# Optimization experiments

Hardware: AMD Instinct MI355X
Metric: run time of the kernel (lower is better)

The kernel has to match this reference:

```python
import jax, jax.numpy as jnp
import numpy as np

HEADS = 8
SCALE_BASE = 512
EPS = 1e-5


def xpos(x, downscale=False):
    # x: (B, h, S, hd) ; XPOS rotary embedding with exponential scale
    hd = x.shape[-1]
    S = x.shape[-2]
    half = hd // 2
    base_scale = (jnp.arange(0, hd, 2, dtype=jnp.float32) + 0.4 * hd) / (1.4 * hd)  # (half,)
    pos = jnp.arange(S, dtype=jnp.float32)
    scale = base_scale[None, :] ** (pos[:, None] / SCALE_BASE)  # (S, half)
    inv_freq = 1.0 / (10000.0 ** (jnp.arange(half, dtype=jnp.float32) / half))
    sinu = pos[:, None] * inv_freq[None, :]  # (S, half)
    sin, cos = jnp.sin(sinu), jnp.cos(sinu)
    if downscale:
        scale = 1.0 / scale
    # duplicate_interleave: (S, half) -> (S, hd)
    sin_s = jnp.repeat(sin * scale, 2, axis=-1)
    cos_s = jnp.repeat(cos * scale, 2, axis=-1)
    x1 = x[..., ::2]
    x2 = x[..., 1::2]
    rot = jnp.stack((-x2, x1), axis=-1).reshape(x.shape)  # rotate_every_two
    return x * cos_s + rot * sin_s


def decay_mask(S):
    # (heads, S, S): gamma^(n-m) for n>=m else 0
    gammas = 1.0 - jnp.exp(jnp.linspace(np.log(1 / 32), np.log(1 / 512), HEADS)).astype(jnp.float32)
    n = jnp.arange(S, dtype=jnp.float32)
    diff = n[:, None] - n[None, :]
    lg = jnp.log(gammas)[:, None, None]
    return jnp.where(diff >= 0, jnp.exp(jnp.maximum(diff, 0.0) * lg), 0.0)


def layer_norm(x, w, b):
    mu = x.mean(-1, keepdims=True)
    var = x.var(-1, keepdims=True)
    return (x - mu) / jnp.sqrt(var + EPS) * w + b


def multiscale_retention(Xq, Xkv, Wq, Wk, Wv, Wg, Wo, gn_w, gn_b):
    # Xq: (B,S,d) query source; Xkv: (B,S,d) key/value source (== Xq for self)
    B, S, _ = Xq.shape
    Q = jnp.einsum('bsd,hde->bhse', Xq, Wq)
    K = jnp.einsum('btd,hde->bhte', Xkv, Wk)
    V = jnp.einsum('btd,hdv->bhtv', Xkv, Wv)
    Q = xpos(Q)
    K = xpos(K, downscale=True)
    D = decay_mask(S)  # (h,S,S)
    scores = jnp.einsum('bhse,bhte->bhst', Q, K) * D[None]
    Y = jnp.einsum('bhst,bhtv->bhsv', scores, V)  # (B,h,S,hv)
    h, hv = Y.shape[1], Y.shape[3]
    # GroupNorm(heads, v_dim) over each head's channels per token
    mu = Y.mean(-1, keepdims=True)
    var = Y.var(-1, keepdims=True)
    Yn = (Y - mu) / jnp.sqrt(var + EPS)
    Yn = Yn.transpose(0, 2, 1, 3).reshape(B, S, h * hv) * gn_w + gn_b
    gate = jax.nn.sigmoid(Xq @ Wg) * (Xq @ Wg)  # swish gate
    return (gate * Yn) @ Wo


def setup_inputs() -> dict:
    key = jax.random.key(0)
    ks = jax.random.split(key, 32)
    d, f, h, hd, hv, vd = 1024, 4096, 8, 128, 256, 2048
    B, S = 2, 2048
    inp = {
        'X': jax.random.normal(ks[0], (B, S, d), jnp.float32),
        'mem': jax.random.normal(ks[1], (B, S, d), jnp.float32),
        'ln1_w': jax.random.uniform(ks[2], (d,), jnp.float32, 0.5, 1.5),
        'ln1_b': jax.random.normal(ks[3], (d,), jnp.float32) * 0.1,
        'ln2_w': jax.random.uniform(ks[4], (d,), jnp.float32, 0.5, 1.5),
        'ln2_b': jax.random.normal(ks[5], (d,), jnp.float32) * 0.1,
        'Wq': jax.random.normal(ks[6], (h, d, hd), jnp.float32) / d,
        'Wk': jax.random.normal(ks[7], (h, d, hd), jnp.float32) / d,
        'Wv': jax.random.normal(ks[8], (h, d, hv), jnp.float32) / d,
        'Wg': jax.random.normal(ks[9], (d, vd), jnp.float32) / d,
        'Wo': jax.random.normal(ks[10], (vd, d), jnp.float32) / d,
        'gn_w': jax.random.uniform(ks[11], (vd,), jnp.float32, 0.5, 1.5),
        'gn_b': jax.random.normal(ks[12], (vd,), jnp.float32) * 0.1,
        'cWq': jax.random.normal(ks[13], (h, d, hd), jnp.float32) / d,
        'cWk': jax.random.normal(ks[14], (h, d, hd), jnp.float32) / d,
        'cWv': jax.random.normal(ks[15], (h, d, hv), jnp.float32) / d,
        'cWg': jax.random.normal(ks[16], (d, vd), jnp.float32) / d,
        'cWo': jax.random.normal(ks[17], (vd, d), jnp.float32) / d,
        'cgn_w': jax.random.uniform(ks[18], (vd,), jnp.float32, 0.5, 1.5),
        'cgn_b': jax.random.normal(ks[19], (vd,), jnp.float32) * 0.1,
        'W1': jax.random.normal(ks[20], (d, f), jnp.float32) * (1.0 / np.sqrt(d)),
        'b1': jax.random.normal(ks[21], (f,), jnp.float32) * 0.02,
        'W2': jax.random.normal(ks[22], (f, d), jnp.float32) * (1.0 / np.sqrt(f)),
        'b2': jax.random.normal(ks[23], (d,), jnp.float32) * 0.02,
    }
    return inp


def reference(X, mem, ln1_w, ln1_b, ln2_w, ln2_b, Wq, Wk, Wv, Wg, Wo, gn_w, gn_b,
              cWq, cWk, cWv, cWg, cWo, cgn_w, cgn_b, W1, b1, W2, b2):
    # self retention block
    X = multiscale_retention(layer_norm(X, ln1_w, ln1_b), None, Wq, Wk, Wv, Wg, Wo, gn_w, gn_b) + X if False else multiscale_retention(layer_norm(X, ln1_w, ln1_b), layer_norm(X, ln1_w, ln1_b), Wq, Wk, Wv, Wg, Wo, gn_w, gn_b) + X
    # cross retention block (note: original reuses layer_norms_2 for both this and the FFN)
    h2 = layer_norm(X, ln2_w, ln2_b)
    X = multiscale_retention(h2, mem, cWq, cWk, cWv, cWg, cWo, cgn_w, cgn_b) + X
    # FFN block (GELU exact, per torch nn.GELU default)
    h3 = layer_norm(X, ln2_w, ln2_b)
    X = (jax.nn.gelu(h3 @ W1 + b1, approximate=False) @ W2 + b2) + X
    return X
```

## Files before the change

kernel.cpp:

```cpp
#include <hip/hip_runtime.h>
#include <math.h>

#define RTOT 4096
#define SEQQ 2048

typedef unsigned int uint32;
typedef __attribute__((ext_vector_type(4))) float f32x4;
typedef __attribute__((ext_vector_type(8))) short bf16x8;

__device__ __forceinline__ unsigned short f2bf(float f) {
  unsigned int u = __float_as_uint(f);
  u = (u + 0x7FFFu + ((u >> 16) & 1u)) >> 16;
  return (unsigned short)u;
}
__device__ __forceinline__ float bf2f(unsigned short h) {
  return __uint_as_float(((unsigned int)h) << 16);
}
__device__ __forceinline__ void gld16(const void* g, void* l) {
  __builtin_amdgcn_global_load_lds(
      (const __attribute__((address_space(1))) uint32*)g,
      (__attribute__((address_space(3))) uint32*)l, 16, 0, 0);
}
__device__ __forceinline__ void bar() {
  asm volatile("" ::: "memory");
  __builtin_amdgcn_s_barrier();
  asm volatile("" ::: "memory");
}
#define VMCNT(n) asm volatile("s_waitcnt vmcnt(" #n ")" ::: "memory")

__global__ __launch_bounds__(256) void transpose_bf16(
    const float* __restrict__ in, unsigned short* __restrict__ out, int R, int C,
    int perm) {
  __shared__ float t[32][33];
  int z = blockIdx.z;
  in  += (size_t)z * R * C;
  out += (size_t)z * C * R;
  int r0 = blockIdx.x * 32, c0 = blockIdx.y * 32;
  int tx = threadIdx.x & 31, ty = threadIdx.x >> 5;
  #pragma unroll
  for (int i = 0; i < 4; ++i) {
    int r = ty + i * 8;
    t[r][tx] = in[(size_t)(r0 + r) * C + c0 + tx];
  }
  __syncthreads();
  #pragma unroll
  for (int i = 0; i < 4; ++i) {
    int cc = c0 + ty + i * 8;
    if (perm) cc = 64 * (cc >> 6) + ((cc & 1) << 5) + ((cc & 63) >> 1);
    out[(size_t)cc * R + r0 + tx] = f2bf(t[tx][ty + i * 8]);
  }
}

__global__ __launch_bounds__(256) void cvt_bf16(
    const float* __restrict__ in, unsigned short* __restrict__ out, int n8) {
  int i = blockIdx.x * 256 + threadIdx.x;
  if (i >= n8) return;
  const float4* p = (const float4*)(in + (size_t)i * 8);
  float4 a = p[0], b = p[1];
  bf16x8 v;
  v[0] = (short)f2bf(a.x); v[1] = (short)f2bf(a.y); v[2] = (short)f2bf(a.z); v[3] = (short)f2bf(a.w);
  v[4] = (short)f2bf(b.x); v[5] = (short)f2bf(b.y); v[6] = (short)f2bf(b.z); v[7] = (short)f2bf(b.w);
  *(bf16x8*)(out + (size_t)i * 8) = v;
}

__global__ __launch_bounds__(256) void tabgen(float* __restrict__ tab) {
  int i = blockIdx.x * 256 + threadIdx.x;
  int pos = i >> 6, j = i & 63;
  float bs = (2.f * (float)j + 51.2f) * (1.f / 179.2f);
  float e = (float)pos * (1.f / 512.f);
  float sc = exp2f(e * log2f(bs));
  float invf = exp2f(-(float)j * (13.287712379549449f / 64.f));
  float su, cu;
  sincosf((float)pos * invf, &su, &cu);
  tab[i]            = cu * sc;
  tab[131072 + i]   = su * sc;
  float si = 1.f / sc;
  tab[262144 + i]   = cu * si;
  tab[393216 + i]   = su * si;
}

__global__ __launch_bounds__(256) void ln_bf16(const float* __restrict__ x,
    const float* __restrict__ w, const float* __restrict__ b,
    unsigned short* __restrict__ out) {
  int row = blockIdx.x, tid = threadIdx.x;
  const float* xr = x + (size_t)row * 1024;
  float4 v = *(const float4*)(xr + tid * 4);
  float s  = v.x + v.y + v.z + v.w;
  float ss = v.x*v.x + v.y*v.y + v.z*v.z + v.w*v.w;
  #pragma unroll
  for (int o = 32; o > 0; o >>= 1) { s += __shfl_down(s, o); ss += __shfl_down(ss, o); }
  __shared__ float red[2][4];
  int wid = tid >> 6;
  if ((tid & 63) == 0) { red[0][wid] = s; red[1][wid] = ss; }
  __syncthreads();
  float st  = red[0][0] + red[0][1] + red[0][2] + red[0][3];
  float sst = red[1][0] + red[1][1] + red[1][2] + red[1][3];
  float mu   = st * (1.f / 1024.f);
  float var  = sst * (1.f / 1024.f) - mu * mu;
  float rstd = rsqrtf(var + 1e-5f);
  float4 wv = *(const float4*)(w + tid * 4);
  float4 bv = *(const float4*)(b + tid * 4);
  unsigned short o0 = f2bf((v.x - mu) * rstd * wv.x + bv.x);
  unsigned short o1 = f2bf((v.y - mu) * rstd * wv.y + bv.y);
  unsigned short o2 = f2bf((v.z - mu) * rstd * wv.z + bv.z);
  unsigned short o3 = f2bf((v.w - mu) * rstd * wv.w + bv.w);
  ushort4 o4 = make_ushort4(o0, o1, o2, o3);
  *(ushort4*)(out + (size_t)row * 1024 + tid * 4) = o4;
}

enum { EPI_F32_RES = 0, EPI_BF16 = 1, EPI_XPOS = 2, EPI_GELU = 4, EPI_BRES = 5,
       EPI_QKG = 6, EPI_QG = 7 };

struct EpiP {
  void* C; int ldc;
  const float* bias; const float* resid;
  const float* tab;
  unsigned short* oQ; unsigned short* oK; unsigned short* oG;
};

template<int EPI>
__device__ __forceinline__ void epi_store(size_t m, int n, int N0, float v, const EpiP& P) {
  if constexpr (EPI == EPI_BF16) {
    ((unsigned short*)P.C)[m * P.ldc + n] = f2bf(v);
  } else if constexpr (EPI == EPI_GELU) {
    v += P.bias[n];
    v = 0.5f * v * (1.f + erff(v * 0.70710678f));
    ((unsigned short*)P.C)[m * P.ldc + n] = f2bf(v);
  } else if constexpr (EPI == EPI_BRES) {
    v += P.bias[n] + P.resid[m * P.ldc + n];
    ((float*)P.C)[m * P.ldc + n] = v;
  } else {
    v += P.resid[m * P.ldc + n];
    ((float*)P.C)[m * P.ldc + n] = v;
  }
}

template<int EPI>
__global__ __launch_bounds__(256) void gemm_mfma(
    const unsigned short* __restrict__ A, int lda,
    const unsigned short* __restrict__ Bt, int ldb, int K, int nbx, EpiP P) {
  __shared__ __align__(16) unsigned short As[2][128 * 32];
  __shared__ __align__(16) unsigned short Bs[2][128 * 32];
  const int tid = threadIdx.x, w = tid >> 6, lane = tid & 63;
  int q8 = (int)gridDim.x >> 3;
  int sbid = ((int)blockIdx.x & 7) * q8 + ((int)blockIdx.x >> 3);
  int by = sbid / nbx, bx = sbid - by * nbx;
  const int M0 = by * 128, N0 = bx * 128;
  const int fr = lane & 15, fs = lane >> 4;
  const int srow = lane >> 2, sp = lane & 3;

  f32x4 zf = {0.f, 0.f, 0.f, 0.f};
  f32x4 acc[4][4];
  #pragma unroll
  for (int i = 0; i < 4; ++i)
    #pragma unroll
    for (int j = 0; j < 4; ++j) acc[i][j] = zf;

  auto STAGE = [&](int buf, int k0) {
    #pragma unroll
    for (int c = 0; c < 4; ++c) {
      int ch = w * 4 + c;
      int cc = ch & 7;
      int row = cc * 16 + srow;
      int so = sp ^ ((row >> 1) & 3);
      if (ch < 8) gld16(A  + (size_t)(M0 + row) * lda + k0 + so * 8, &As[buf][cc * 512]);
      else        gld16(Bt + (size_t)(N0 + row) * ldb + k0 + so * 8, &Bs[buf][cc * 512]);
    }
  };

  STAGE(0, 0);
  int cur = 0;
  for (int k0 = 0; k0 < K; k0 += 32) {
    if (k0 + 32 < K) { STAGE(cur ^ 1, k0 + 32); VMCNT(4); }
    else             { VMCNT(0); }
    bar();
    bf16x8 af[4], bfr[4];
    #pragma unroll
    for (int mi = 0; mi < 4; ++mi) {
      int row = (w >> 1) * 64 + mi * 16 + fr;
      af[mi] = *(const bf16x8*)(&As[cur][row * 32 + (fs ^ ((row >> 1) & 3)) * 8]);
    }
    #pragma unroll
    for (int ni = 0; ni < 4; ++ni) {
      int row = (w & 1) * 64 + ni * 16 + fr;
      bfr[ni] = *(const bf16x8*)(&Bs[cur][row * 32 + (fs ^ ((row >> 1) & 3)) * 8]);
    }
    #pragma unroll
    for (int mi = 0; mi < 4; ++mi)
      #pragma unroll
      for (int ni = 0; ni < 4; ++ni)
        acc[mi][ni] = __builtin_amdgcn_mfma_f32_16x16x32_bf16(af[mi], bfr[ni], acc[mi][ni], 0, 0, 0);
    bar();
    cur ^= 1;
  }

  #pragma unroll
  for (int mi = 0; mi < 4; ++mi)
    #pragma unroll
    for (int r = 0; r < 4; ++r) {
      size_t m = M0 + (w >> 1) * 64 + mi * 16 + fs * 4 + r;
      #pragma unroll
      for (int ni = 0; ni < 4; ++ni) {
        int n = N0 + (w & 1) * 64 + ni * 16 + fr;
        epi_store<EPI>(m, n, N0, acc[mi][ni][r], P);
      }
    }
}

template<int EPI>
__global__ __launch_bounds__(256) void gemm_bn64(
    const unsigned short* __restrict__ A, int lda,
    const unsigned short* __restrict__ Bt, int ldb, int K, int nbx, EpiP P) {
  __shared__ __align__(16) unsigned short As[2][128 * 32];
  __shared__ __align__(16) unsigned short Bs[2][64 * 32];
  const int tid = threadIdx.x, w = tid >> 6, lane = tid & 63;
  int q8 = (int)gridDim.x >> 3;
  int sbid = ((int)blockIdx.x & 7) * q8 + ((int)blockIdx.x >> 3);
  int by = sbid / nbx, bx = sbid - by * nbx;
  const int M0 = by * 128, N0 = bx * 64;
  const int fr = lane & 15, fs = lane >> 4;
  const int srow = lane >> 2, sp = lane & 3;

  f32x4 zf = {0.f, 0.f, 0.f, 0.f};
  f32x4 acc[2][4];
  #pragma unroll
  for (int i = 0; i < 2; ++i)
    #pragma unroll
    for (int j = 0; j < 4; ++j) acc[i][j] = zf;

  auto STAGE = [&](int buf, int k0) {
    #pragma unroll
    for (int c = 0; c < 3; ++c) {
      int ch = w * 3 + c;
      if (ch < 8) {
        int row = ch * 16 + srow;
        int so = sp ^ ((row >> 1) & 3);
        gld16(A + (size_t)(M0 + row) * lda + k0 + so * 8, &As[buf][ch * 512]);
      } else {
        int bch = ch - 8;
        int row = bch * 16 + srow;
        int so = sp ^ ((row >> 1) & 3);
        gld16(Bt + (size_t)(N0 + row) * ldb + k0 + so * 8, &Bs[buf][bch * 512]);
      }
    }
  };

  STAGE(0, 0);
  int cur = 0;
  for (int k0 = 0; k0 < K; k0 += 32) {
    if (k0 + 32 < K) { STAGE(cur ^ 1, k0 + 32); VMCNT(3); }
    else             { VMCNT(0); }
    bar();
    bf16x8 af[2], bfr[4];
    #pragma unroll
    for (int mi = 0; mi < 2; ++mi) {
      int row = w * 32 + mi * 16 + fr;
      af[mi] = *(const bf16x8*)(&As[cur][row * 32 + (fs ^ ((row >> 1) & 3)) * 8]);
    }
    #pragma unroll
    for (int ni = 0; ni < 4; ++ni) {
      int row = ni * 16 + fr;
      bfr[ni] = *(const bf16x8*)(&Bs[cur][row * 32 + (fs ^ ((row >> 1) & 3)) * 8]);
    }
    #pragma unroll
    for (int mi = 0; mi < 2; ++mi)
      #pragma unroll
      for (int ni = 0; ni < 4; ++ni)
        acc[mi][ni] = __builtin_amdgcn_mfma_f32_16x16x32_bf16(af[mi], bfr[ni], acc[mi][ni], 0, 0, 0);
    bar();
    cur ^= 1;
  }

  if constexpr (EPI == EPI_XPOS) {
    int gsel = (N0 >> 6) & 1;
    #pragma unroll
    for (int mi = 0; mi < 2; ++mi)
      #pragma unroll
      for (int r = 0; r < 4; ++r) {
        size_t m = M0 + w * 32 + mi * 16 + fs * 4 + r;
        int pos = (int)(m & (SEQQ - 1));
        #pragma unroll
        for (int ni = 0; ni < 2; ++ni) {
          int j = gsel * 32 + ni * 16 + fr;
          float cs = P.tab[pos * 64 + j], sn = P.tab[131072 + pos * 64 + j];
          float ve = acc[mi][ni][r], vo = acc[mi][ni + 2][r];
          unsigned short* dst = (unsigned short*)P.C;
          dst[m * P.ldc + N0 + ni * 16 + fr]       = f2bf(ve * cs - vo * sn);
          dst[m * P.ldc + N0 + (ni + 2) * 16 + fr] = f2bf(vo * cs + ve * sn);
        }
      }
  } else {
    #pragma unroll
    for (int mi = 0; mi < 2; ++mi)
      #pragma unroll
      for (int r = 0; r < 4; ++r) {
        size_t m = M0 + w * 32 + mi * 16 + fs * 4 + r;
        #pragma unroll
        for (int ni = 0; ni < 4; ++ni) {
          int n = N0 + ni * 16 + fr;
          epi_store<EPI>(m, n, N0, acc[mi][ni][r], P);
        }
      }
  }
}

template<int EPI>
__global__ __launch_bounds__(512, 2) void gemm256(
    const unsigned short* __restrict__ A,
    const unsigned short* __restrict__ Bt,
    int nbx, EpiP P) {
  __shared__ __align__(16) unsigned short lds[4][2][8192];
  const int tid = threadIdx.x, w = tid >> 6, lane = tid & 63;
  int cpx = (int)gridDim.x >> 3;
  int sbid = ((int)blockIdx.x & 7) * cpx + ((int)blockIdx.x >> 3);
  int by = sbid / nbx, bx = sbid - by * nbx;
  const int M0 = by * 256, N0 = bx * 256;
  const int wm = w >> 2, wn = w & 3;
  const int fr = lane & 15, fs = lane >> 4;
  const int srow = lane >> 2;
  const int sslot = (lane & 3) ^ ((lane >> 3) & 3);
  const int rsw = (fr >> 1) & 3;

  f32x4 acc[8][4];
  #pragma unroll
  for (int i = 0; i < 8; ++i)
    #pragma unroll
    for (int j = 0; j < 4; ++j) acc[i][j] = {0.f, 0.f, 0.f, 0.f};

  auto STAGE = [&](int t, int buf) {
    int k0 = t * 32;
    #pragma unroll
    for (int j = 0; j < 4; ++j) {
      int c = w * 4 + j;
      if (c < 16)
        gld16(A  + (size_t)(M0 + c * 16 + srow) * 1024 + k0 + sslot * 8,
              &lds[buf][0][c * 512]);
      else
        gld16(Bt + (size_t)(N0 + (c - 16) * 16 + srow) * 1024 + k0 + sslot * 8,
              &lds[buf][1][(c - 16) * 512]);
    }
  };
  auto COMPUTE = [&](int t) {
    const unsigned short* la = &lds[t & 3][0][wm * 128 * 32];
    const unsigned short* lb = &lds[t & 3][1][wn * 64 * 32];
    bf16x8 a[8], b[4];
    #pragma unroll
    for (int ni = 0; ni < 4; ++ni)
      b[ni] = *(const bf16x8*)(lb + (ni * 16 + fr) * 32 + ((fs ^ rsw) * 8));
    #pragma unroll
    for (int mi = 0; mi < 8; ++mi)
      a[mi] = *(const bf16x8*)(la + (mi * 16 + fr) * 32 + ((fs ^ rsw) * 8));
    #pragma unroll
    for (int mi = 0; mi < 8; ++mi)
      #pragma unroll
      for (int ni = 0; ni < 4; ++ni)
        acc[mi][ni] = __builtin_amdgcn_mfma_f32_16x16x32_bf16(a[mi], b[ni], acc[mi][ni], 0, 0, 0);
  };

  STAGE(0, 0); STAGE(1, 1); STAGE(2, 2);
  for (int t = 0; t < 29; ++t) {
    STAGE(t + 3, (t + 3) & 3);
    VMCNT(12);
    bar();
    COMPUTE(t);
    bar();
  }
  VMCNT(8);  bar(); COMPUTE(29); bar();
  VMCNT(4);  bar(); COMPUTE(30); bar();
  VMCNT(0);  bar(); COMPUTE(31);

  if constexpr (EPI == EPI_GELU) {
    #pragma unroll
    for (int mi = 0; mi < 8; ++mi)
      #pragma unroll
      for (int r = 0; r < 4; ++r) {
        size_t m = M0 + wm * 128 + mi * 16 + fs * 4 + r;
        #pragma unroll
        for (int ni = 0; ni < 4; ++ni) {
          int n = N0 + wn * 64 + ni * 16 + fr;
          float v = acc[mi][ni][r] + P.bias[n];
          v = 0.5f * v * (1.f + erff(v * 0.70710678f));
          ((unsigned short*)P.C)[m * P.ldc + n] = f2bf(v);
        }
      }
  } else {
    const int nb = N0 + wn * 64;
    const bool isQ = nb < 1024;
    const bool isK = (EPI == EPI_QKG) && !isQ && (nb < 2048);
    if (isQ || isK) {
      const float* tc = isK ? P.tab + 262144 : P.tab;
      const float* ts = tc + 131072;
      unsigned short* dst = isK ? P.oK : P.oQ;
      const int nloc = isK ? nb - 1024 : nb;
      const int gsel = (nloc >> 6) & 1;
      #pragma unroll
      for (int mi = 0; mi < 8; ++mi)
        #pragma unroll
        for (int r = 0; r < 4; ++r) {
          size_t m = M0 + wm * 128 + mi * 16 + fs * 4 + r;
          int pos = (int)(m & (SEQQ - 1));
          #pragma unroll
          for (int ni = 0; ni < 2; ++ni) {
            int j = gsel * 32 + ni * 16 + fr;
            float cs = tc[pos * 64 + j], sn = ts[pos * 64 + j];
            float ve = acc[mi][ni][r], vo = acc[mi][ni + 2][r];
            dst[m * 1024 + nloc + ni * 16 + fr]       = f2bf(ve * cs - vo * sn);
            dst[m * 1024 + nloc + (ni + 2) * 16 + fr] = f2bf(vo * cs + ve * sn);
          }
        }
    } else {
      const int nloc = nb - ((EPI == EPI_QKG) ? 2048 : 1024);
      #pragma unroll
      for (int mi = 0; mi < 8; ++mi)
        #pragma unroll
        for (int r = 0; r < 4; ++r) {
          size_t m = M0 + wm * 128 + mi * 16 + fs * 4 + r;
          #pragma unroll
          for (int ni = 0; ni < 4; ++ni) {
            float v = acc[mi][ni][r];
            P.oG[m * 2048 + nloc + ni * 16 + fr] = f2bf(v / (1.f + expf(-v)));
          }
        }
    }
  }
}

__global__ __launch_bounds__(256) void retention_mfma(
    const unsigned short* __restrict__ Qx, const unsigned short* __restrict__ Kx,
    const unsigned short* __restrict__ VT, const unsigned short* __restrict__ Gate,
    const float* __restrict__ gnw, const float* __restrict__ gnb,
    unsigned short* __restrict__ Gout) {
  __shared__ __align__(16) unsigned short Ks[2][32 * 128];
  __shared__ __align__(16) unsigned short Vs[2][256 * 32];
  const int tid = threadIdx.x, w = tid >> 6, lane = tid & 63;
  int bid = blockIdx.x, qt, h, b;
  if (bid < 256) { qt = 31 - (bid >> 3); h = bid & 7; b = 0; }
  else           { int k = bid - 256; qt = k >> 3; h = k & 7; b = 1; }
  const int q0 = qt * 64;
  const int fr = lane & 15, fs = lane >> 4;

  float gamma = 1.f - expf(-3.4657359028f - 0.3960841032f * (float)h);
  float l2g = log2f(gamma);
  const int qglob = q0 + w * 16 + fr;

  size_t qrow = (size_t)b * SEQQ + qglob;
  bf16x8 qf[4];
  #pragma unroll
  for (int ks = 0; ks < 4; ++ks)
    qf[ks] = *(const bf16x8*)(Qx + qrow * 1024 + h * 128 + ks * 32 + fs * 8);

  float gtl8[8];
  #pragma unroll
  for (int i = 0; i < 8; ++i) {
    int toff = (i >> 2) * 16 + fs * 4 + (i & 3);
    gtl8[i] = exp2f(-(float)toff * l2g);
  }

  f32x4 zf = {0.f, 0.f, 0.f, 0.f};
  f32x4 yacc[16];
  #pragma unroll
  for (int i = 0; i < 16; ++i) yacc[i] = zf;

  int cutoff = (int)(27.f / (-l2g));
  int t_start = q0 - cutoff;
  if (t_start < 0) t_start = 0;
  t_start &= ~31;
  size_t kbase = (size_t)b * SEQQ;

  auto STAGE = [&](int buf, int t0) {
    #pragma unroll
    for (int c = 0; c < 2; ++c) {
      int ch = w * 2 + c;
      int row = ch * 4 + (lane >> 4);
      int so = (lane & 15) ^ (row & 15);
      gld16(Kx + (kbase + t0 + row) * 1024 + h * 128 + so * 8, &Ks[buf][ch * 512]);
    }
    #pragma unroll
    for (int c = 0; c < 4; ++c) {
      int ch = w * 4 + c;
      int vrow = ch * 16 + (lane >> 2);
      int so = (lane & 3) ^ ((vrow >> 1) & 3);
      gld16(VT + (size_t)(h * 256 + vrow) * RTOT + kbase + t0 + so * 8, &Vs[buf][ch * 512]);
    }
  };

  STAGE(0, t_start);
  int cur = 0;
  for (int t0 = t_start; t0 < q0 + 64; t0 += 32) {
    if (t0 + 32 < q0 + 64) { STAGE(cur ^ 1, t0 + 32); VMCNT(6); }
    else                   { VMCNT(0); }
    bar();

    f32x4 sacc[2];
    sacc[0] = zf; sacc[1] = zf;
    #pragma unroll
    for (int nt = 0; nt < 2; ++nt) {
      int row = nt * 16 + fr;
      #pragma unroll
      for (int ks = 0; ks < 4; ++ks) {
        int sl = ks * 4 + fs;
        bf16x8 kf = *(const bf16x8*)(&Ks[cur][row * 128 + (sl ^ (row & 15)) * 8]);
        sacc[nt] = __builtin_amdgcn_mfma_f32_16x16x32_bf16(kf, qf[ks], sacc[nt], 0, 0, 0);
      }
    }
    float fsc = exp2f((float)(qglob - t0) * l2g);
    uint32 pk[4];
    #pragma unroll
    for (int nt = 0; nt < 2; ++nt)
      #pragma unroll
      for (int hf = 0; hf < 2; ++hf) {
        int r0i = hf * 2;
        int ta = t0 + nt * 16 + fs * 4 + r0i;
        float va = (qglob >= ta)     ? sacc[nt][r0i]     * (fsc * gtl8[nt * 4 + r0i])     : 0.f;
        float vb = (qglob >= ta + 1) ? sacc[nt][r0i + 1] * (fsc * gtl8[nt * 4 + r0i + 1]) : 0.f;
        pk[nt * 2 + hf] = (uint32)f2bf(va) | ((uint32)f2bf(vb) << 16);
      }
    union { uint32 u[4]; bf16x8 v8; } pa;
    #pragma unroll
    for (int j = 0; j < 4; ++j) {
      int src = fr + 16 * (2 * (fs & 1) + (j >> 1));
      int v0 = __shfl((int)pk[j & 1],     src);
      int v1 = __shfl((int)pk[2 + (j & 1)], src);
      pa.u[j] = (fs < 2) ? (uint32)v0 : (uint32)v1;
    }
    #pragma unroll
    for (int nv = 0; nv < 16; ++nv) {
      int vrow = nv * 16 + fr;
      bf16x8 vf = *(const bf16x8*)(&Vs[cur][vrow * 32 + (fs ^ ((vrow >> 1) & 3)) * 8]);
      yacc[nv] = __builtin_amdgcn_mfma_f32_16x16x32_bf16(pa.v8, vf, yacc[nv], 0, 0, 0);
    }
    bar();
    cur ^= 1;
  }

  #pragma unroll
  for (int r = 0; r < 4; ++r) {
    float s = 0.f, sq = 0.f;
    #pragma unroll
    for (int nv = 0; nv < 16; ++nv) { float v = yacc[nv][r]; s += v; sq += v * v; }
    #pragma unroll
    for (int msk = 1; msk < 16; msk <<= 1) { s += __shfl_xor(s, msk); sq += __shfl_xor(sq, msk); }
    float mu = s * (1.f / 256.f);
    float var = sq * (1.f / 256.f) - mu * mu;
    float rstd = rsqrtf(var + 1e-5f);
    int srow = q0 + w * 16 + fs * 4 + r;
    size_t mrow = (size_t)b * SEQQ + srow;
    const unsigned short* grow = Gate + mrow * 2048 + h * 256;
    unsigned short* orow = Gout + mrow * 2048 + h * 256;
    #pragma unroll
    for (int nv = 0; nv < 16; ++nv) {
      int col = nv * 16 + fr;
      float yn = (yacc[nv][r] - mu) * rstd * gnw[h * 256 + col] + gnb[h * 256 + col];
      orow[col] = f2bf(bf2f(grow[col]) * yn);
    }
  }
}

extern "C" void kernel_launch(void* const* d_in, const int* in_sizes, int n_in,
                              void* d_out, int out_size, void* d_ws, size_t ws_size,
                              hipStream_t stream) {
  const float* X    = (const float*)d_in[0];
  const float* mem  = (const float*)d_in[1];
  const float* ln1w = (const float*)d_in[2];
  const float* ln1b = (const float*)d_in[3];
  const float* ln2w = (const float*)d_in[4];
  const float* ln2b = (const float*)d_in[5];
  const float* Wq   = (const float*)d_in[6];
  const float* Wk   = (const float*)d_in[7];
  const float* Wv   = (const float*)d_in[8];
  const float* Wg   = (const float*)d_in[9];
  const float* Wo   = (const float*)d_in[10];
  const float* gnw  = (const float*)d_in[11];
  const float* gnb  = (const float*)d_in[12];
  const float* cWq  = (const float*)d_in[13];
  const float* cWk  = (const float*)d_in[14];
  const float* cWv  = (const float*)d_in[15];
  const float* cWg  = (const float*)d_in[16];
  const float* cWo  = (const float*)d_in[17];
  const float* cgnw = (const float*)d_in[18];
  const float* cgnb = (const float*)d_in[19];
  const float* W1   = (const float*)d_in[20];
  const float* b1   = (const float*)d_in[21];
  const float* W2   = (const float*)d_in[22];
  const float* b2   = (const float*)d_in[23];
  float* out = (float*)d_out;

  const size_t MB = 1024ull * 1024ull;
  if (ws_size < 106 * MB) return;
  unsigned char* W8 = (unsigned char*)d_ws;
  unsigned short* WqkgT = (unsigned short*)(W8 + 0 * MB);
  unsigned short* WvT   = (unsigned short*)(W8 + 8 * MB);
  unsigned short* WoT   = (unsigned short*)(W8 + 12 * MB);
  unsigned short* cQGT  = (unsigned short*)(W8 + 16 * MB);
  unsigned short* cWkT  = (unsigned short*)(W8 + 22 * MB);
  unsigned short* cWvT  = (unsigned short*)(W8 + 24 * MB);
  unsigned short* cWoT  = (unsigned short*)(W8 + 28 * MB);
  float*          tab   = (float*)(W8 + 32 * MB);
  unsigned short* hbuf  = (unsigned short*)(W8 + 34 * MB);
  unsigned short* Qx    = (unsigned short*)(W8 + 42 * MB);
  unsigned short* Kx    = (unsigned short*)(W8 + 50 * MB);
  unsigned short* W1T   = Qx;
  unsigned short* W2T   = Kx;
  unsigned short* VTb   = (unsigned short*)(W8 + 58 * MB);
  unsigned short* Gg    = (unsigned short*)(W8 + 74 * MB);
  unsigned short* Tb    = VTb;
  unsigned short* GoutB = (unsigned short*)(W8 + 90 * MB);
  unsigned short* mem16 = GoutB;

  transpose_bf16<<<dim3(32, 4, 8),  256, 0, stream>>>(Wq,  WqkgT,               1024, 128, 1);
  transpose_bf16<<<dim3(32, 4, 8),  256, 0, stream>>>(Wk,  WqkgT + 1024 * 1024, 1024, 128, 1);
  transpose_bf16<<<dim3(32, 64, 1), 256, 0, stream>>>(Wg,  WqkgT + 2048 * 1024, 1024, 2048, 0);
  transpose_bf16<<<dim3(32, 8, 8),  256, 0, stream>>>(Wv,  WvT,  1024, 256, 0);
  transpose_bf16<<<dim3(64, 32, 1), 256, 0, stream>>>(Wo,  WoT,  2048, 1024, 0);
  transpose_bf16<<<dim3(32, 4, 8),  256, 0, stream>>>(cWq, cQGT,               1024, 128, 1);
  transpose_bf16<<<dim3(32, 64, 1), 256, 0, stream>>>(cWg, cQGT + 1024 * 1024, 1024, 2048, 0);
  transpose_bf16<<<dim3(32, 4, 8),  256, 0, stream>>>(cWk, cWkT, 1024, 128, 1);
  transpose_bf16<<<dim3(32, 8, 8),  256, 0, stream>>>(cWv, cWvT, 1024, 256, 0);
  transpose_bf16<<<dim3(64, 32, 1), 256, 0, stream>>>(cWo, cWoT, 2048, 1024, 0);
  tabgen<<<512, 256, 0, stream>>>(tab);

  EpiP P{};

  ln_bf16<<<RTOT, 256, 0, stream>>>(X, ln1w, ln1b, hbuf);
  P = EpiP{nullptr, 0, nullptr, nullptr, tab, Qx, Kx, Gg};
  gemm256<EPI_QKG><<<256, 512, 0, stream>>>(hbuf, WqkgT, 16, P);
  P = EpiP{VTb, 4096, nullptr, nullptr, nullptr, nullptr, nullptr, nullptr};
  gemm_mfma<EPI_BF16><<<512, 256, 0, stream>>>(WvT, 1024, hbuf, 1024, 1024, 32, P);
  retention_mfma<<<dim3(512), 256, 0, stream>>>(Qx, Kx, VTb, Gg, gnw, gnb, GoutB);
  P = EpiP{out, 1024, nullptr, X, nullptr, nullptr, nullptr, nullptr};
  gemm_bn64<EPI_F32_RES><<<512, 256, 0, stream>>>(GoutB, 2048, WoT, 2048, 2048, 16, P);

  cvt_bf16<<<2048, 256, 0, stream>>>(mem, mem16, 524288);
  ln_bf16<<<RTOT, 256, 0, stream>>>(out, ln2w, ln2b, hbuf);
  P = EpiP{nullptr, 0, nullptr, nullptr, tab, Qx, nullptr, Gg};
  gemm256<EPI_QG><<<192, 512, 0, stream>>>(hbuf, cQGT, 12, P);
  P = EpiP{Kx, 1024, nullptr, nullptr, tab + 262144, nullptr, nullptr, nullptr};
  gemm_bn64<EPI_XPOS><<<512, 256, 0, stream>>>(mem16, 1024, cWkT, 1024, 1024, 16, P);
  P = EpiP{VTb, 4096, nullptr, nullptr, nullptr, nullptr, nullptr, nullptr};
  gemm_mfma<EPI_BF16><<<512, 256, 0, stream>>>(cWvT, 1024, mem16, 1024, 1024, 32, P);
  retention_mfma<<<dim3(512), 256, 0, stream>>>(Qx, Kx, VTb, Gg, cgnw, cgnb, GoutB);
  P = EpiP{out, 1024, nullptr, out, nullptr, nullptr, nullptr, nullptr};
  gemm_bn64<EPI_F32_RES><<<512, 256, 0, stream>>>(GoutB, 2048, cWoT, 2048, 2048, 16, P);

  transpose_bf16<<<dim3(32, 128, 1), 256, 0, stream>>>(W1, W1T, 1024, 4096, 0);
  transpose_bf16<<<dim3(128, 32, 1), 256, 0, stream>>>(W2, W2T, 4096, 1024, 0);
  ln_bf16<<<RTOT, 256, 0, stream>>>(out, ln2w, ln2b, hbuf);
  P = EpiP{Tb, 4096, b1, nullptr, nullptr, nullptr, nullptr, nullptr};
  gemm256<EPI_GELU><<<256, 512, 0, stream>>>(hbuf, W1T, 16, P);
  P = EpiP{out, 1024, b2, out, nullptr, nullptr, nullptr, nullptr};
  gemm_bn64<EPI_BRES><<<512, 256, 0, stream>>>(Tb, 4096, W2T, 4096, 4096, 16, P);
}
```

Measured before the change: 570.6 us.

## Split retention key range across two blocks and combine with separate groupnorm kernel

Each retention tile's key loop is split into two halves handled by separate blocks (1024 blocks instead of 512). Each half writes an unnormalized bf16 partial Y. A new combine kernel sums the partials and applies groupnorm and the gate. This is meant to fix load imbalance and low occupancy from the causal triangle. In exchange it adds extra global traffic, an extra launch, and bf16 rounding of the partials. Weight-transpose launches are reordered so their workspace regions can be reused for the partial buffers.

```diff
diff --git a/kernel.cpp b/kernel.cpp
--- a/kernel.cpp
+++ b/kernel.cpp
@@ -425,17 +425,19 @@
   }
 }
 
-__global__ __launch_bounds__(256) void retention_mfma(
+__global__ __launch_bounds__(256) void retention_part(
     const unsigned short* __restrict__ Qx, const unsigned short* __restrict__ Kx,
-    const unsigned short* __restrict__ VT, const unsigned short* __restrict__ Gate,
-    const float* __restrict__ gnw, const float* __restrict__ gnb,
-    unsigned short* __restrict__ Gout) {
+    const unsigned short* __restrict__ VT,
+    unsigned short* __restrict__ Y0, unsigned short* __restrict__ Y1) {
   __shared__ __align__(16) unsigned short Ks[2][32 * 128];
   __shared__ __align__(16) unsigned short Vs[2][256 * 32];
   const int tid = threadIdx.x, w = tid >> 6, lane = tid & 63;
-  int bid = blockIdx.x, qt, h, b;
-  if (bid < 256) { qt = 31 - (bid >> 3); h = bid & 7; b = 0; }
-  else           { int k = bid - 256; qt = k >> 3; h = k & 7; b = 1; }
+  int bid = blockIdx.x;
+  int th = bid >> 9;
+  int rr = bid & 511;
+  int qt, h, b;
+  if (rr < 256) { qt = 31 - (rr >> 3); h = rr & 7; b = 0; }
+  else          { int k = rr - 256; qt = k >> 3; h = k & 7; b = 1; }
   const int q0 = qt * 64;
   const int fr = lane & 15, fs = lane >> 4;
 
@@ -484,11 +486,18 @@
     }
   };
 
-  STAGE(0, t_start);
+  const int nt_total = (q0 + 64 - t_start) >> 5;
+  const int n0 = (nt_total + 1) >> 1;
+  const int it0 = th ? n0 : 0;
+  const int it1 = th ? nt_total : n0;
+  unsigned short* Yp = th ? Y1 : Y0;
+
+  STAGE(0, t_start + it0 * 32);
   int cur = 0;
-  for (int t0 = t_start; t0 < q0 + 64; t0 += 32) {
-    if (t0 + 32 < q0 + 64) { STAGE(cur ^ 1, t0 + 32); VMCNT(6); }
-    else                   { VMCNT(0); }
+  for (int it = it0; it < it1; ++it) {
+    int t0 = t_start + it * 32;
+    if (it + 1 < it1) { STAGE(cur ^ 1, t0 + 32); VMCNT(6); }
+    else              { VMCNT(0); }
     bar();
 
     f32x4 sacc[2];
@@ -535,25 +544,48 @@
 
   #pragma unroll
   for (int r = 0; r < 4; ++r) {
-    float s = 0.f, sq = 0.f;
-    #pragma unroll
-    for (int nv = 0; nv < 16; ++nv) { float v = yacc[nv][r]; s += v; sq += v * v; }
-    #pragma unroll
-    for (int msk = 1; msk < 16; msk <<= 1) { s += __shfl_xor(s, msk); sq += __shfl_xor(sq, msk); }
-    float mu = s * (1.f / 256.f);
-    float var = sq * (1.f / 256.f) - mu * mu;
-    float rstd = rsqrtf(var + 1e-5f);
     int srow = q0 + w * 16 + fs * 4 + r;
     size_t mrow = (size_t)b * SEQQ + srow;
-    const unsigned short* grow = Gate + mrow * 2048 + h * 256;
-    unsigned short* orow = Gout + mrow * 2048 + h * 256;
-    #pragma unroll
-    for (int nv = 0; nv < 16; ++nv) {
-      int col = nv * 16 + fr;
-      float yn = (yacc[nv][r] - mu) * rstd * gnw[h * 256 + col] + gnb[h * 256 + col];
-      orow[col] = f2bf(bf2f(grow[col]) * yn);
-    }
-  }
+    unsigned short* orow = Yp + mrow * 2048 + h * 256;
+    #pragma unroll
+    for (int nv = 0; nv < 16; ++nv)
+      orow[nv * 16 + fr] = f2bf(yacc[nv][r]);
+  }
+}
+
+__global__ __launch_bounds__(256) void combine_gn(
+    const unsigned short* __restrict__ Y0, const unsigned short* __restrict__ Y1,
+    const unsigned short* __restrict__ Gate,
+    const float* __restrict__ gnw, const float* __restrict__ gnb,
+    unsigned short* __restrict__ Gout) {
+  int idx = blockIdx.x * 4 + (threadIdx.x >> 6);
+  int lane = threadIdx.x & 63;
+  int h = idx & 7;
+  size_t row = (size_t)(idx >> 3);
+  size_t base = row * 2048 + h * 256 + lane * 4;
+  ushort4 a = *(const ushort4*)(Y0 + base);
+  ushort4 bb = *(const ushort4*)(Y1 + base);
+  float y0 = bf2f(a.x) + bf2f(bb.x);
+  float y1 = bf2f(a.y) + bf2f(bb.y);
+  float y2 = bf2f(a.z) + bf2f(bb.z);
+  float y3 = bf2f(a.w) + bf2f(bb.w);
+  float s  = y0 + y1 + y2 + y3;
+  float sq = y0*y0 + y1*y1 + y2*y2 + y3*y3;
+  #pragma unroll
+  for (int o = 32; o > 0; o >>= 1) { s += __shfl_xor(s, o); sq += __shfl_xor(sq, o); }
+  float mu = s * (1.f / 256.f);
+  float var = sq * (1.f / 256.f) - mu * mu;
+  float rstd = rsqrtf(var + 1e-5f);
+  int gi = h * 256 + lane * 4;
+  float4 w4 = *(const float4*)(gnw + gi);
+  float4 b4 = *(const float4*)(gnb + gi);
+  ushort4 g4 = *(const ushort4*)(Gate + base);
+  ushort4 o4;
+  o4.x = f2bf(bf2f(g4.x) * ((y0 - mu) * rstd * w4.x + b4.x));
+  o4.y = f2bf(bf2f(g4.y) * ((y1 - mu) * rstd * w4.y + b4.y));
+  o4.z = f2bf(bf2f(g4.z) * ((y2 - mu) * rstd * w4.z + b4.z));
+  o4.w = f2bf(bf2f(g4.w) * ((y3 - mu) * rstd * w4.w + b4.w));
+  *(ushort4*)(Gout + base) = o4;
 }
 
 extern "C" void kernel_launch(void* const* d_in, const int* in_sizes, int n_in,
@@ -606,29 +638,33 @@
   unsigned short* Tb    = VTb;
   unsigned short* GoutB = (unsigned short*)(W8 + 90 * MB);
   unsigned short* mem16 = GoutB;
+  unsigned short* Yp1a  = (unsigned short*)(W8 + 16 * MB);
+  unsigned short* Yp1b  = (unsigned short*)(W8 + 0 * MB);
 
   transpose_bf16<<<dim3(32, 4, 8),  256, 0, stream>>>(Wq,  WqkgT,               1024, 128, 1);
   transpose_bf16<<<dim3(32, 4, 8),  256, 0, stream>>>(Wk,  WqkgT + 1024 * 1024, 1024, 128, 1);
   transpose_bf16<<<dim3(32, 64, 1), 256, 0, stream>>>(Wg,  WqkgT + 2048 * 1024, 1024, 2048, 0);
   transpose_bf16<<<dim3(32, 8, 8),  256, 0, stream>>>(Wv,  WvT,  1024, 256, 0);
   transpose_bf16<<<dim3(64, 32, 1), 256, 0, stream>>>(Wo,  WoT,  2048, 1024, 0);
+  tabgen<<<512, 256, 0, stream>>>(tab);
+
+  EpiP P{};
+
+  ln_bf16<<<RTOT, 256, 0, stream>>>(X, ln1w, ln1b, hbuf);
+  P = EpiP{nullptr, 0, nullptr, nullptr, tab, Qx, Kx, Gg};
+  gemm256<EPI_QKG><<<256, 512, 0, stream>>>(hbuf, WqkgT, 16, P);
+  P = EpiP{VTb, 4096, nullptr, nullptr, nullptr, nullptr, nullptr, nullptr};
+  gemm_mfma<EPI_BF16><<<512, 256, 0, stream>>>(WvT, 1024, hbuf, 1024, 1024, 32, P);
+  retention_part<<<dim3(1024), 256, 0, stream>>>(Qx, Kx, VTb, GoutB, Yp1a);
+  combine_gn<<<RTOT * 2, 256, 0, stream>>>(GoutB, Yp1a, Gg, gnw, gnb, GoutB);
+  P = EpiP{out, 1024, nullptr, X, nullptr, nullptr, nullptr, nullptr};
+  gemm_bn64<EPI_F32_RES><<<512, 256, 0, stream>>>(GoutB, 2048, WoT, 2048, 2048, 16, P);
+
   transpose_bf16<<<dim3(32, 4, 8),  256, 0, stream>>>(cWq, cQGT,               1024, 128, 1);
   transpose_bf16<<<dim3(32, 64, 1), 256, 0, stream>>>(cWg, cQGT + 1024 * 1024, 1024, 2048, 0);
   transpose_bf16<<<dim3(32, 4, 8),  256, 0, stream>>>(cWk, cWkT, 1024, 128, 1);
   transpose_bf16<<<dim3(32, 8, 8),  256, 0, stream>>>(cWv, cWvT, 1024, 256, 0);
   transpose_bf16<<<dim3(64, 32, 1), 256, 0, stream>>>(cWo, cWoT, 2048, 1024, 0);
-  tabgen<<<512, 256, 0, stream>>>(tab);
-
-  EpiP P{};
-
-  ln_bf16<<<RTOT, 256, 0, stream>>>(X, ln1w, ln1b, hbuf);
-  P = EpiP{nullptr, 0, nullptr, nullptr, tab, Qx, Kx, Gg};
-  gemm256<EPI_QKG><<<256, 512, 0, stream>>>(hbuf, WqkgT, 16, P);
-  P = EpiP{VTb, 4096, nullptr, nullptr, nullptr, nullptr, nullptr, nullptr};
-  gemm_mfma<EPI_BF16><<<512, 256, 0, stream>>>(WvT, 1024, hbuf, 1024, 1024, 32, P);
-  retention_mfma<<<dim3(512), 256, 0, stream>>>(Qx, Kx, VTb, Gg, gnw, gnb, GoutB);
-  P = EpiP{out, 1024, nullptr, X, nullptr, nullptr, nullptr, nullptr};
-  gemm_bn64<EPI_F32_RES><<<512, 256, 0, stream>>>(GoutB, 2048, WoT, 2048, 2048, 16, P);
 
   cvt_bf16<<<2048, 256, 0, stream>>>(mem, mem16, 524288);
   ln_bf16<<<RTOT, 256, 0, stream>>>(out, ln2w, ln2b, hbuf);
@@ -638,7 +674,8 @@
   gemm_bn64<EPI_XPOS><<<512, 256, 0, stream>>>(mem16, 1024, cWkT, 1024, 1024, 16, P);
   P = EpiP{VTb, 4096, nullptr, nullptr, nullptr, nullptr, nullptr, nullptr};
   gemm_mfma<EPI_BF16><<<512, 256, 0, stream>>>(cWvT, 1024, mem16, 1024, 1024, 32, P);
-  retention_mfma<<<dim3(512), 256, 0, stream>>>(Qx, Kx, VTb, Gg, cgnw, cgnb, GoutB);
+  retention_part<<<dim3(1024), 256, 0, stream>>>(Qx, Kx, VTb, GoutB, Yp1b);
+  combine_gn<<<RTOT * 2, 256, 0, stream>>>(GoutB, Yp1b, Gg, cgnw, cgnb, GoutB);
   P = EpiP{out, 1024, nullptr, out, nullptr, nullptr, nullptr, nullptr};
   gemm_bn64<EPI_F32_RES><<<512, 256, 0, stream>>>(GoutB, 2048, cWoT, 2048, 2048, 16, P);
 
```

After: 558.1 us. 2.2% less time.
